# Performance work log

Measured on AMD Instinct MI355X. Metric: run time of the kernel, lower is better.

The kernel has to match this reference:

```python
import jax, jax.numpy as jnp
import numpy as np

B, S, E, H, DH = 4, 2048, 2048, 16, 256  # DH = mlp hidden (d_hid)
HD = E // H  # per-head dim = 128
EPS = 1e-5

def _ln(x, w, b):
    m = jnp.mean(x, axis=-1, keepdims=True)
    v = jnp.mean(jnp.square(x - m), axis=-1, keepdims=True)
    return (x - m) * jax.lax.rsqrt(v + EPS) * w + b

def setup_inputs() -> dict:
    key = jax.random.key(0)
    ks = jax.random.split(key, 10)
    s = 0.02
    return {
        "x": jax.random.normal(ks[0], (B, S, E), jnp.float32),
        "attention_mask": jax.random.randint(ks[1], (B, S), 0, 2, jnp.int32),
        "ln1_w": jnp.ones((E,), jnp.float32),
        "ln1_b": jnp.zeros((E,), jnp.float32),
        "in_proj_w": jax.random.normal(ks[2], (3 * E, E), jnp.float32) * s,
        "in_proj_b": jnp.zeros((3 * E,), jnp.float32),
        "out_proj_w": jax.random.normal(ks[3], (E, E), jnp.float32) * s,
        "out_proj_b": jnp.zeros((E,), jnp.float32),
        "ln2_w": jnp.ones((E,), jnp.float32),
        "ln2_b": jnp.zeros((E,), jnp.float32),
        "mlp_w1": jax.random.normal(ks[4], (DH, E), jnp.float32) * s,
        "mlp_b1": jnp.zeros((DH,), jnp.float32),
        "mlp_w2": jax.random.normal(ks[5], (E, DH), jnp.float32) * s,
        "mlp_b2": jnp.zeros((E,), jnp.float32),
    }

def reference(x, attention_mask, ln1_w, ln1_b, in_proj_w, in_proj_b,
              out_proj_w, out_proj_b, ln2_w, ln2_b, mlp_w1, mlp_b1, mlp_w2, mlp_b2):
    h = _ln(x, ln1_w, ln1_b)
    qkv = h @ in_proj_w.T + in_proj_b  # [B,S,3E]
    q, k, v = jnp.split(qkv, 3, axis=-1)
    q = q.reshape(B, S, H, HD).transpose(0, 2, 1, 3) / jnp.sqrt(jnp.float32(HD))
    k = k.reshape(B, S, H, HD).transpose(0, 2, 1, 3)
    v = v.reshape(B, S, H, HD).transpose(0, 2, 1, 3)
    scores = jnp.einsum("bhqd,bhkd->bhqk", q, k)
    # Faithful to source: FLOAT attn_mask of +1.0 on strictly-upper triangle (additive),
    # NOT -inf; key_padding_mask positions do get -inf.
    causal_add = jnp.triu(jnp.ones((S, S), jnp.float32), k=1)
    scores = scores + causal_add
    pad = (attention_mask == 0)  # True = padded key
    scores = jnp.where(pad[:, None, None, :], jnp.float32(-jnp.inf), scores)
    attn = jax.nn.softmax(scores, axis=-1)
    ctx = jnp.einsum("bhqk,bhkd->bhqd", attn, v)
    ctx = ctx.transpose(0, 2, 1, 3).reshape(B, S, E)
    x = x + ctx @ out_proj_w.T + out_proj_b
    h2 = _ln(x, ln2_w, ln2_b)
    mlp = jax.nn.relu(h2 @ mlp_w1.T + mlp_b1) @ mlp_w2.T + mlp_b2
    return x + mlp
```

## Files before the change

### kernel.cpp

```cpp
#include <hip/hip_runtime.h>

typedef __attribute__((ext_vector_type(8))) short short8;
typedef __attribute__((ext_vector_type(4))) float f32x4;
typedef __attribute__((ext_vector_type(16))) float f32x16;

typedef __attribute__((address_space(1))) const void gas1_t;
typedef __attribute__((address_space(3))) void las3_t;
#define GLL16(g, l) __builtin_amdgcn_global_load_lds((gas1_t*)(g), (las3_t*)(l), 16, 0, 0)

__device__ inline unsigned short f2bf(float f) {
  union { float f; unsigned int u; } v; v.f = f;
  unsigned int r = v.u + 0x7FFFu + ((v.u >> 16) & 1u);
  return (unsigned short)(r >> 16);
}

__device__ inline float exp2_fast(float x) {
  float r; asm("v_exp_f32 %0, %1" : "=v"(r) : "v"(x)); return r;
}

__device__ inline void vmwait(int n) {
  if (n == 6)      asm volatile("s_waitcnt vmcnt(6)" ::: "memory");
  else             asm volatile("s_waitcnt vmcnt(0)" ::: "memory");
}

__global__ __launch_bounds__(256) void ln_kernel(const float* __restrict__ x,
                                                 const float* __restrict__ w,
                                                 const float* __restrict__ bia,
                                                 unsigned short* __restrict__ out) {
  const int row = blockIdx.x;
  const int tid = threadIdx.x;
  const float* xr = x + (size_t)row * 2048;
  float4 a = *(const float4*)(xr + tid * 8);
  float4 b = *(const float4*)(xr + tid * 8 + 4);
  float s  = a.x + a.y + a.z + a.w + b.x + b.y + b.z + b.w;
  float s2 = a.x*a.x + a.y*a.y + a.z*a.z + a.w*a.w + b.x*b.x + b.y*b.y + b.z*b.z + b.w*b.w;
  #pragma unroll
  for (int off = 1; off < 64; off <<= 1) {
    s  += __shfl_xor(s, off);
    s2 += __shfl_xor(s2, off);
  }
  __shared__ float red[8];
  if ((tid & 63) == 0) { red[tid >> 6] = s; red[4 + (tid >> 6)] = s2; }
  __syncthreads();
  s  = red[0] + red[1] + red[2] + red[3];
  s2 = red[4] + red[5] + red[6] + red[7];
  const float mean = s * (1.f / 2048.f);
  const float var  = s2 * (1.f / 2048.f) - mean * mean;
  const float rstd = rsqrtf(var + 1e-5f);
  float4 wa = *(const float4*)(w + tid * 8), wb = *(const float4*)(w + tid * 8 + 4);
  float4 ba = *(const float4*)(bia + tid * 8), bb = *(const float4*)(bia + tid * 8 + 4);
  short8 o;
  o[0] = (short)f2bf((a.x - mean) * rstd * wa.x + ba.x);
  o[1] = (short)f2bf((a.y - mean) * rstd * wa.y + ba.y);
  o[2] = (short)f2bf((a.z - mean) * rstd * wa.z + ba.z);
  o[3] = (short)f2bf((a.w - mean) * rstd * wa.w + ba.w);
  o[4] = (short)f2bf((b.x - mean) * rstd * wb.x + bb.x);
  o[5] = (short)f2bf((b.y - mean) * rstd * wb.y + bb.y);
  o[6] = (short)f2bf((b.z - mean) * rstd * wb.z + bb.z);
  o[7] = (short)f2bf((b.w - mean) * rstd * wb.w + bb.w);
  *(short8*)(out + (size_t)row * 2048 + tid * 8) = o;
}

__global__ __launch_bounds__(256) void conv_kernel(const float* __restrict__ in,
                                                   unsigned short* __restrict__ out, int n) {
  size_t idx = ((size_t)blockIdx.x * 256 + threadIdx.x) * 8;
  if (idx >= (size_t)n) return;
  float4 a = *(const float4*)(in + idx);
  float4 b = *(const float4*)(in + idx + 4);
  short8 o;
  o[0] = (short)f2bf(a.x); o[1] = (short)f2bf(a.y);
  o[2] = (short)f2bf(a.z); o[3] = (short)f2bf(a.w);
  o[4] = (short)f2bf(b.x); o[5] = (short)f2bf(b.y);
  o[6] = (short)f2bf(b.z); o[7] = (short)f2bf(b.w);
  *(short8*)(out + idx) = o;
}

template <int MODE>
__global__ __launch_bounds__(256) void gemm_bt(const unsigned short* __restrict__ A,
                                               const unsigned short* __restrict__ Bw,
                                               const float* __restrict__ bias,
                                               const float* __restrict__ res,
                                               void* __restrict__ outp,
                                               void* __restrict__ outp2,
                                               int M, int N, int K) {
  __shared__ unsigned short As[128 * 64];
  __shared__ unsigned short Bs[128 * 64];
  const int tid = threadIdx.x;
  const int l = tid & 63, wv = tid >> 6;
  const int l15 = l & 15, l4 = l >> 4;
  const int wr = wv >> 1, wc = wv & 1;
  const int nx = gridDim.x;
  const int nwg = nx * gridDim.y;
  const int bidlin = blockIdx.y * nx + blockIdx.x;
  const int cpx = nwg >> 3;
  const int swz = (bidlin & 7) * cpx + (bidlin >> 3);
  const int m0 = (swz / nx) * 128, n0 = (swz % nx) * 128;

  f32x4 acc[4][4] = {};
  for (int k0 = 0; k0 < K; k0 += 64) {
    __syncthreads();
    #pragma unroll
    for (int i = 0; i < 4; ++i) {
      int e = i * 2048 + tid * 8;
      int r = e >> 6;
      int c = (e ^ ((r & 7) << 3)) & 63;
      GLL16(A + (size_t)(m0 + r) * K + k0 + c, As + e);
      GLL16(Bw + (size_t)(n0 + r) * K + k0 + c, Bs + e);
    }
    __syncthreads();
    #pragma unroll
    for (int kk = 0; kk < 64; kk += 32) {
      short8 af[4], bfr[4];
      #pragma unroll
      for (int m = 0; m < 4; ++m) {
        int r = wr * 64 + m * 16 + l15;
        int byt = (r * 128 + (kk + l4 * 8) * 2) ^ ((r & 7) << 4);
        af[m] = *(const short8*)((const char*)As + byt);
      }
      #pragma unroll
      for (int n = 0; n < 4; ++n) {
        int r = wc * 64 + n * 16 + l15;
        int byt = (r * 128 + (kk + l4 * 8) * 2) ^ ((r & 7) << 4);
        bfr[n] = *(const short8*)((const char*)Bs + byt);
      }
      #pragma unroll
      for (int m = 0; m < 4; ++m)
        #pragma unroll
        for (int n = 0; n < 4; ++n)
          acc[m][n] = __builtin_amdgcn_mfma_f32_16x16x32_bf16(af[m], bfr[n], acc[m][n], 0, 0, 0);
    }
  }
  #pragma unroll
  for (int m = 0; m < 4; ++m) {
    #pragma unroll
    for (int n = 0; n < 4; ++n) {
      #pragma unroll
      for (int r = 0; r < 4; ++r) {
        int row = m0 + wr * 64 + m * 16 + l4 * 4 + r;
        int col = n0 + wc * 64 + n * 16 + l15;
        float v = acc[m][n][r] + bias[col];
        if (MODE == 1) {
          ((unsigned short*)outp)[(size_t)row * N + col] = f2bf(v > 0.f ? v : 0.f);
        } else {
          ((float*)outp)[(size_t)row * N + col] = res[(size_t)row * N + col] + v;
        }
      }
    }
  }
}

template <int MODE>
__global__ __launch_bounds__(512, 2) void gemm8(const unsigned short* __restrict__ A,
                                                const unsigned short* __restrict__ Bw,
                                                const float* __restrict__ bias,
                                                const float* __restrict__ res,
                                                void* __restrict__ outp,
                                                void* __restrict__ outp2,
                                                int M, int N, int K) {
  __shared__ char LA[2][2][16384];
  __shared__ char LB[2][2][16384];
  const int tid = threadIdx.x;
  const int l = tid & 63, wv = tid >> 6;
  const int l15 = l & 15, l4 = l >> 4;
  const int wr = wv >> 2, wc = wv & 3;
  const int wch = wc >> 1, wcl = wc & 1;
  const int nx = gridDim.x;
  const int nwg = nx * gridDim.y;
  const int bidlin = blockIdx.y * nx + blockIdx.x;
  const int cpx = nwg >> 3;
  const int swz = (bidlin & 7) * cpx + (bidlin >> 3);
  const int m0 = (swz / nx) * 256, n0 = (swz % nx) * 256;

  const int srow = tid >> 3;
  const int scol = ((tid & 7) ^ (srow & 7)) * 8;

#define STG_A(x, h) { const unsigned short* bp = A + (size_t)(m0 + (h) * 128) * K + (x) * 64; \
    GLL16(bp + (size_t)srow * K + scol, &LA[(x) & 1][h][tid * 16]); \
    GLL16(bp + (size_t)(srow + 64) * K + scol, &LA[(x) & 1][h][8192 + tid * 16]); }
#define STG_B(x, h) { const unsigned short* bp = Bw + (size_t)(n0 + (h) * 128) * K + (x) * 64; \
    GLL16(bp + (size_t)srow * K + scol, &LB[(x) & 1][h][tid * 16]); \
    GLL16(bp + (size_t)(srow + 64) * K + scol, &LB[(x) & 1][h][8192 + tid * 16]); }

#define FOFF(r, kh) ((r) * 128 + (((((kh) * 4 + l4)) ^ ((r) & 7)) << 4))

  f32x4 acc[8][4] = {};
  const int NT = K >> 6;

  STG_A(0, 0); STG_A(0, 1); STG_B(0, 0); STG_B(0, 1);
  STG_B(1, 0); STG_B(1, 1); STG_A(1, 0);
  vmwait(6);
  __builtin_amdgcn_s_barrier();

#define MFMAQ(mh, nh) \
    __builtin_amdgcn_s_setprio(1); \
    _Pragma("unroll") for (int kh = 0; kh < 2; ++kh) \
      _Pragma("unroll") for (int f = 0; f < 4; ++f) \
        _Pragma("unroll") for (int n = 0; n < 2; ++n) \
          acc[(mh) * 4 + f][(nh) * 2 + n] = __builtin_amdgcn_mfma_f32_16x16x32_bf16( \
              af[kh][f], bfr[kh][(nh) * 2 + n], acc[(mh) * 4 + f][(nh) * 2 + n], 0, 0, 0); \
    __builtin_amdgcn_s_setprio(0);

  for (int t = 0; t < NT; ++t) {
    const char* Ab = LA[t & 1][wr];
    const char* Bb = LB[t & 1][wch];
    short8 af[2][4], bfr[2][4];
    #pragma unroll
    for (int kh = 0; kh < 2; ++kh)
      #pragma unroll
      for (int f = 0; f < 4; ++f) {
        af[kh][f] = *(const short8*)(Ab + FOFF(f * 16 + l15, kh));
        bfr[kh][f] = *(const short8*)(Bb + FOFF(wcl * 64 + f * 16 + l15, kh));
      }
    if (t + 1 < NT) STG_A(t + 1, 1);
    __builtin_amdgcn_s_barrier();
    asm volatile("s_waitcnt lgkmcnt(0)" ::: "memory");
    __builtin_amdgcn_sched_barrier(0);
    MFMAQ(0, 0);
    __builtin_amdgcn_s_barrier();
    if (t + 2 < NT) STG_B(t + 2, 0);
    __builtin_amdgcn_s_barrier();
    MFMAQ(0, 1);
    __builtin_amdgcn_s_barrier();
    #pragma unroll
    for (int kh = 0; kh < 2; ++kh)
      #pragma unroll
      for (int f = 0; f < 4; ++f)
        af[kh][f] = *(const short8*)(Ab + FOFF(64 + f * 16 + l15, kh));
    if (t + 2 < NT) STG_B(t + 2, 1);
    __builtin_amdgcn_s_barrier();
    asm volatile("s_waitcnt lgkmcnt(0)" ::: "memory");
    __builtin_amdgcn_sched_barrier(0);
    MFMAQ(1, 0);
    __builtin_amdgcn_s_barrier();
    if (t + 2 < NT) STG_A(t + 2, 0);
    __builtin_amdgcn_s_barrier();
    MFMAQ(1, 1);
    vmwait(t >= NT - 2 ? 0 : 6);
    __builtin_amdgcn_s_barrier();
  }
#undef MFMAQ
#undef FOFF
#undef STG_A
#undef STG_B

  #pragma unroll
  for (int mf = 0; mf < 8; ++mf) {
    #pragma unroll
    for (int nf = 0; nf < 4; ++nf) {
      #pragma unroll
      for (int r = 0; r < 4; ++r) {
        int row = m0 + wr * 128 + mf * 16 + l4 * 4 + r;
        int col = n0 + wc * 64 + nf * 16 + l15;
        float v = acc[mf][nf][r] + bias[col];
        if (MODE == 0) {
          unsigned short val = f2bf(v);
          if (col < 4096) ((unsigned short*)outp)[(size_t)row * 4096 + col] = val;
          else            ((unsigned short*)outp2)[(size_t)row * 2048 + col - 4096] = val;
        } else {
          ((float*)outp)[(size_t)row * N + col] = res[(size_t)row * N + col] + v;
        }
      }
    }
  }
}

__global__ __launch_bounds__(256) void vtrans_kernel(const unsigned short* __restrict__ v,
                                                     unsigned short* __restrict__ vT) {
  __shared__ unsigned short T[128 * 128];
  const int t0 = blockIdx.x * 128;
  const int b = blockIdx.y >> 4, h = blockIdx.y & 15;
  const int tid = threadIdx.x;
  const int tl = tid >> 4, l16 = tid & 15, c8 = l16 * 8;
  #pragma unroll
  for (int i = 0; i < 8; ++i) {
    int t = tl + i * 16;
    short8 val = *(const short8*)(v + (size_t)(b * 2048 + t0 + t) * 2048 + h * 128 + c8);
    *(short8*)((char*)T + ((t * 256 + c8 * 2) ^ ((t & 7) << 4))) = val;
  }
  __syncthreads();
  #pragma unroll
  for (int i = 0; i < 8; ++i) {
    int d = tl + i * 16;
    unsigned short* orow = vT + ((size_t)(b * 16 + h) * 128 + d) * 2048 + t0;
    #pragma unroll
    for (int j = 0; j < 8; ++j) {
      int t = l16 + 16 * j;
      orow[t] = *(const unsigned short*)((const char*)T + ((t * 256 + d * 2) ^ ((t & 7) << 4)));
    }
  }
}

__global__ __launch_bounds__(256) void attn_kernel(const unsigned short* __restrict__ qk,
                                                   const unsigned short* __restrict__ vT,
                                                   const int* __restrict__ amask,
                                                   unsigned short* __restrict__ ctx) {
  __shared__ unsigned short Ks[2][4096];
  __shared__ unsigned short Vs[2][4096];
  __shared__ unsigned short Pl[4][1152];

  const int qt = blockIdx.x, bh = blockIdx.y;
  const int b = bh >> 4, h = bh & 15;
  const int tid = threadIdx.x;
  const int wv = tid >> 6, l = tid & 63;
  const int l31 = l & 31, hi = l >> 5;
  const int q0w = qt * 128 + wv * 32;
  const float SC2 = 0.08838834764831845f * 1.4426950408889634f;
  const float L2E = 1.4426950408889634f;
  const float MF  = 10.0f;

  int kinv[2], vinv[2];
  #pragma unroll
  for (int c = 0; c < 2; ++c) {
    int e = c * 2048 + tid * 8;
    int key = e >> 7, d0 = e & 127;
    kinv[c] = key * 4096 + 2048 + h * 128 + (d0 ^ ((key & 7) << 3));
    int d = e >> 5, kchunk = ((e >> 3) & 3) ^ ((d & 6) >> 1);
    vinv[c] = d * 2048 + kchunk * 8;
  }
  const unsigned short* kb0 = qk + (size_t)(b * 2048) * 4096;
  const unsigned short* vb0 = vT + (size_t)(b * 16 + h) * (128 * 2048);
  const int* mrow = amask + b * 2048;

  short8 qf[8];
  {
    const unsigned short* qp = qk + (size_t)(b * 2048 + q0w + l31) * 4096 + h * 128 + hi * 8;
    #pragma unroll
    for (int c = 0; c < 8; ++c) qf[c] = *(const short8*)(qp + c * 16);
  }

  short8 vones;
  #pragma unroll
  for (int j = 0; j < 8; ++j) vones[j] = (short)0x3F80;

  f32x16 o[4] = {};
  f32x16 ol = {};

  #pragma unroll
  for (int c = 0; c < 2; ++c) {
    GLL16(kb0 + kinv[c], &Ks[0][c * 2048 + tid * 8]);
    GLL16(vb0 + vinv[c], &Vs[0][c * 2048 + tid * 8]);
  }
  __syncthreads();

  for (int kt = 0; kt < 2048; kt += 32) {
    const int cur = (kt >> 5) & 1;
    if (kt + 32 < 2048) {
      #pragma unroll
      for (int c = 0; c < 2; ++c) {
        GLL16(kb0 + (size_t)(kt + 32) * 4096 + kinv[c], &Ks[cur ^ 1][c * 2048 + tid * 8]);
        GLL16(vb0 + (kt + 32) + vinv[c], &Vs[cur ^ 1][c * 2048 + tid * 8]);
      }
    }
    const bool pad = (mrow[kt + l31] == 0);

    f32x16 sacc = {};
    __builtin_amdgcn_s_setprio(1);
    #pragma unroll
    for (int c = 0; c < 8; ++c) {
      short8 kf = *(const short8*)((const char*)Ks[cur] +
                   ((l31 * 256 + c * 32 + hi * 16) ^ ((l31 & 7) << 4)));
      sacc = __builtin_amdgcn_mfma_f32_32x32x16_bf16(qf[c], kf, sacc, 0, 0, 0);
    }
    __builtin_amdgcn_s_setprio(0);

    float s[16];
    if (kt > q0w + 31) {
      #pragma unroll
      for (int i = 0; i < 16; ++i) s[i] = sacc[i] * SC2 + L2E;
    } else if (kt + 31 <= q0w) {
      #pragma unroll
      for (int i = 0; i < 16; ++i) s[i] = sacc[i] * SC2;
    } else {
      int kg = kt + l31;
      #pragma unroll
      for (int i = 0; i < 16; ++i) {
        int qg = q0w + (i & 3) + 8 * (i >> 2) + 4 * hi;
        s[i] = sacc[i] * SC2 + ((kg > qg) ? L2E : 0.f);
      }
    }
    if (pad) {
      #pragma unroll
      for (int i = 0; i < 16; ++i) s[i] = -1e30f;
    }

    #pragma unroll
    for (int i = 0; i < 16; ++i) {
      int q = (i & 3) + 8 * (i >> 2) + 4 * hi;
      Pl[wv][q * 36 + l31] = f2bf(exp2_fast(s[i] - MF));
    }
    short8 pa0 = *(const short8*)&Pl[wv][l31 * 36 + hi * 8];
    short8 pa1 = *(const short8*)&Pl[wv][l31 * 36 + 16 + hi * 8];

    __builtin_amdgcn_s_setprio(1);
    #pragma unroll
    for (int g = 0; g < 4; ++g) {
      int d = g * 32 + l31;
      int swzd = (d & 6) << 3;
      short8 vf0 = *(const short8*)((const char*)Vs[cur] + ((d * 64 + hi * 16) ^ swzd));
      o[g] = __builtin_amdgcn_mfma_f32_32x32x16_bf16(pa0, vf0, o[g], 0, 0, 0);
      short8 vf1 = *(const short8*)((const char*)Vs[cur] + ((d * 64 + 32 + hi * 16) ^ swzd));
      o[g] = __builtin_amdgcn_mfma_f32_32x32x16_bf16(pa1, vf1, o[g], 0, 0, 0);
    }
    ol = __builtin_amdgcn_mfma_f32_32x32x16_bf16(pa0, vones, ol, 0, 0, 0);
    ol = __builtin_amdgcn_mfma_f32_32x32x16_bf16(pa1, vones, ol, 0, 0, 0);
    __builtin_amdgcn_s_setprio(0);

    __syncthreads();
  }

  float inv[16];
  #pragma unroll
  for (int i = 0; i < 16; ++i) inv[i] = 1.0f / ol[i];
  #pragma unroll
  for (int g = 0; g < 4; ++g) {
    #pragma unroll
    for (int i = 0; i < 16; ++i) {
      int q = q0w + (i & 3) + 8 * (i >> 2) + 4 * hi;
      ctx[(size_t)(b * 2048 + q) * 2048 + h * 128 + g * 32 + l31] = f2bf(o[g][i] * inv[i]);
    }
  }
}

extern "C" void kernel_launch(void* const* d_in, const int* in_sizes, int n_in,
                              void* d_out, int out_size, void* d_ws, size_t ws_size,
                              hipStream_t stream) {
  (void)in_sizes; (void)n_in; (void)out_size; (void)ws_size;
  const float* x    = (const float*)d_in[0];
  const int*   am   = (const int*)d_in[1];
  const float* ln1w = (const float*)d_in[2];
  const float* ln1b = (const float*)d_in[3];
  const float* win  = (const float*)d_in[4];
  const float* bin  = (const float*)d_in[5];
  const float* wout = (const float*)d_in[6];
  const float* bout = (const float*)d_in[7];
  const float* ln2w = (const float*)d_in[8];
  const float* ln2b = (const float*)d_in[9];
  const float* w1   = (const float*)d_in[10];
  const float* b1   = (const float*)d_in[11];
  const float* w2   = (const float*)d_in[12];
  const float* b2   = (const float*)d_in[13];
  float* out = (float*)d_out;

  char* ws = (char*)d_ws;
  unsigned short* hbuf = (unsigned short*)ws;
  unsigned short* vTb  = (unsigned short*)ws;
  unsigned short* qkb  = (unsigned short*)(ws + (size_t)32 * 1048576);
  unsigned short* h2b  = (unsigned short*)(ws + (size_t)32 * 1048576);
  unsigned short* midb = (unsigned short*)(ws + (size_t)64 * 1048576);
  unsigned short* vbuf = (unsigned short*)(ws + (size_t)96 * 1048576);
  unsigned short* ctxb = (unsigned short*)(ws + (size_t)96 * 1048576);
  unsigned short* wbuf = (unsigned short*)(ws + (size_t)128 * 1048576);

  ln_kernel<<<dim3(8192), dim3(256), 0, stream>>>(x, ln1w, ln1b, hbuf);
  conv_kernel<<<dim3(6144), dim3(256), 0, stream>>>(win, wbuf, 12582912);
  gemm8<0><<<dim3(24, 32), dim3(512), 0, stream>>>(hbuf, wbuf, bin, (const float*)nullptr,
                                                   (void*)qkb, (void*)vbuf, 8192, 6144, 2048);
  vtrans_kernel<<<dim3(16, 64), dim3(256), 0, stream>>>(vbuf, vTb);
  attn_kernel<<<dim3(16, 64), dim3(256), 0, stream>>>(qkb, vTb, am, ctxb);
  conv_kernel<<<dim3(2048), dim3(256), 0, stream>>>(wout, wbuf, 4194304);
  gemm8<2><<<dim3(8, 32), dim3(512), 0, stream>>>(ctxb, wbuf, bout, x,
                                                  (void*)out, nullptr, 8192, 2048, 2048);
  ln_kernel<<<dim3(8192), dim3(256), 0, stream>>>(out, ln2w, ln2b, h2b);
  conv_kernel<<<dim3(256), dim3(256), 0, stream>>>(w1, wbuf, 524288);
  gemm_bt<1><<<dim3(2, 64), dim3(256), 0, stream>>>(h2b, wbuf, b1, (const float*)nullptr,
                                                    (void*)midb, nullptr, 8192, 256, 2048);
  conv_kernel<<<dim3(256), dim3(256), 0, stream>>>(w2, wbuf, 524288);
  gemm_bt<2><<<dim3(16, 64), dim3(256), 0, stream>>>(midb, wbuf, b2, out,
                                                     (void*)out, nullptr, 8192, 2048, 256);
}
```

Before: 631.2 us.

## Transpose score MFMA, pack P with cvt_pk_bf16, ballot pad mask, swizzle blocks

```diff
diff --git a/kernel.cpp b/kernel.cpp
--- a/kernel.cpp
+++ b/kernel.cpp
@@ -296,9 +296,11 @@
                                                    unsigned short* __restrict__ ctx) {
   __shared__ unsigned short Ks[2][4096];
   __shared__ unsigned short Vs[2][4096];
-  __shared__ unsigned short Pl[4][1152];
-
-  const int qt = blockIdx.x, bh = blockIdx.y;
+  __shared__ char Pl[4][2304];
+
+  const int lin = blockIdx.y * 16 + blockIdx.x;
+  const int swzb = (lin & 7) * 128 + (lin >> 3);
+  const int qt = swzb & 15, bh = swzb >> 4;
   const int b = bh >> 4, h = bh & 15;
   const int tid = threadIdx.x;
   const int wv = tid >> 6, l = tid & 63;
@@ -351,7 +353,8 @@
         GLL16(vb0 + (kt + 32) + vinv[c], &Vs[cur ^ 1][c * 2048 + tid * 8]);
       }
     }
-    const bool pad = (mrow[kt + l31] == 0);
+    const unsigned bm = (unsigned)__ballot((l < 32) && (mrow[kt + l31] == 0));
+    const unsigned bmh = bm >> (4 * hi);
 
     f32x16 sacc = {};
     __builtin_amdgcn_s_setprio(1);
@@ -359,10 +362,11 @@
     for (int c = 0; c < 8; ++c) {
       short8 kf = *(const short8*)((const char*)Ks[cur] +
                    ((l31 * 256 + c * 32 + hi * 16) ^ ((l31 & 7) << 4)));
-      sacc = __builtin_amdgcn_mfma_f32_32x32x16_bf16(qf[c], kf, sacc, 0, 0, 0);
+      sacc = __builtin_amdgcn_mfma_f32_32x32x16_bf16(kf, qf[c], sacc, 0, 0, 0);
     }
     __builtin_amdgcn_s_setprio(0);
 
+    const int Dq = q0w + l31 - kt - 4 * hi;
     float s[16];
     if (kt > q0w + 31) {
       #pragma unroll
@@ -371,25 +375,31 @@
       #pragma unroll
       for (int i = 0; i < 16; ++i) s[i] = sacc[i] * SC2;
     } else {
-      int kg = kt + l31;
       #pragma unroll
       for (int i = 0; i < 16; ++i) {
-        int qg = q0w + (i & 3) + 8 * (i >> 2) + 4 * hi;
-        s[i] = sacc[i] * SC2 + ((kg > qg) ? L2E : 0.f);
-      }
-    }
-    if (pad) {
-      #pragma unroll
-      for (int i = 0; i < 16; ++i) s[i] = -1e30f;
-    }
-
+        const int ci = (i & 3) + 8 * (i >> 2);
+        s[i] = sacc[i] * SC2 + ((ci > Dq) ? L2E : 0.f);
+      }
+    }
     #pragma unroll
     for (int i = 0; i < 16; ++i) {
-      int q = (i & 3) + 8 * (i >> 2) + 4 * hi;
-      Pl[wv][q * 36 + l31] = f2bf(exp2_fast(s[i] - MF));
-    }
-    short8 pa0 = *(const short8*)&Pl[wv][l31 * 36 + hi * 8];
-    short8 pa1 = *(const short8*)&Pl[wv][l31 * 36 + 16 + hi * 8];
+      const int ci = (i & 3) + 8 * (i >> 2);
+      if ((bmh >> ci) & 1) s[i] = -1e30f;
+    }
+
+    float p[16];
+    #pragma unroll
+    for (int i = 0; i < 16; ++i) p[i] = exp2_fast(s[i] - MF);
+    char* prow = &Pl[wv][l31 * 72 + 8 * hi];
+    #pragma unroll
+    for (int j = 0; j < 8; ++j) {
+      const int Kj = ((2 * j) & 3) + 8 * ((2 * j) >> 2);
+      unsigned pk;
+      asm("v_cvt_pk_bf16_f32 %0, %1, %2" : "=v"(pk) : "v"(p[2 * j]), "v"(p[2 * j + 1]));
+      *(unsigned*)(prow + 2 * Kj) = pk;
+    }
+    short8 pa0 = *(const short8*)(&Pl[wv][l31 * 72 + 16 * hi]);
+    short8 pa1 = *(const short8*)(&Pl[wv][l31 * 72 + 32 + 16 * hi]);
 
     __builtin_amdgcn_s_setprio(1);
     #pragma unroll
```

After: 615.3 us. 1.03x faster.
